# Kernel optimization log

Hardware: AMD Instinct MI355X
Metric: run time of the kernel (lower is better)

The kernel has to match this reference:

```python
import jax, jax.numpy as jnp
import numpy as np

NUM_HEADS = 16
NUM_KV_HEADS = 4
HEAD_DIM = 64
HIDDEN = 1024
B, S = 2, 2048


def setup_inputs() -> dict:
    key = jax.random.key(0)
    ks = jax.random.split(key, 9)
    sc = 0.02
    return {
        "x": jax.random.normal(ks[0], (B, S, HIDDEN), dtype=jnp.float32),
        "Wq": jax.random.normal(ks[1], (HIDDEN, NUM_HEADS * HEAD_DIM), dtype=jnp.float32) * sc,
        "bq": jnp.zeros((NUM_HEADS * HEAD_DIM,), dtype=jnp.float32),
        "Wk": jax.random.normal(ks[2], (HIDDEN, NUM_KV_HEADS * HEAD_DIM), dtype=jnp.float32) * sc,
        "bk": jnp.zeros((NUM_KV_HEADS * HEAD_DIM,), dtype=jnp.float32),
        "Wv": jax.random.normal(ks[3], (HIDDEN, NUM_KV_HEADS * HEAD_DIM), dtype=jnp.float32) * sc,
        "bv": jnp.zeros((NUM_KV_HEADS * HEAD_DIM,), dtype=jnp.float32),
        "Wo": jax.random.normal(ks[4], (NUM_HEADS * HEAD_DIM, HIDDEN), dtype=jnp.float32) * sc,
        "bo": jnp.zeros((HIDDEN,), dtype=jnp.float32),
    }


def reference(x, Wq, bq, Wk, bk, Wv, bv, Wo, bo):
    bs, seq, _ = x.shape
    groups = NUM_HEADS // NUM_KV_HEADS
    # projections -> [B, H, S, D]
    q = (x @ Wq + bq).reshape(bs, seq, NUM_HEADS, HEAD_DIM).transpose(0, 2, 1, 3)
    k = (x @ Wk + bk).reshape(bs, seq, NUM_KV_HEADS, HEAD_DIM).transpose(0, 2, 1, 3)
    v = (x @ Wv + bv).reshape(bs, seq, NUM_KV_HEADS, HEAD_DIM).transpose(0, 2, 1, 3)
    # repeat_interleave KV heads to match query heads (GQA expansion)
    k = jnp.repeat(k, groups, axis=1)
    v = jnp.repeat(v, groups, axis=1)
    # NOTE: source applies NO 1/sqrt(d) scaling and no mask/ALiBi
    scores = jnp.einsum("bhqd,bhkd->bhqk", q, k)
    attn = jax.nn.softmax(scores.astype(jnp.float32), axis=-1).astype(q.dtype)
    out = jnp.einsum("bhqk,bhkd->bhqd", attn, v)
    out = out.transpose(0, 2, 1, 3).reshape(bs, seq, NUM_HEADS * HEAD_DIM)
    return out @ Wo + bo
```

## Files before the change

kernel.cpp:

```cpp
#include <hip/hip_runtime.h>

#define NHEADS 16
#define NKV    4
#define HDIM   64
#define HIDDEN 1024
#define BATCH  2
#define SEQ    2048
#define MROWS  (BATCH * SEQ)
#define LOG2E  1.44269504088896340736f

typedef __bf16 bf16_t;
typedef bf16_t bf16x8 __attribute__((ext_vector_type(8)));
typedef float  f32x4  __attribute__((ext_vector_type(4)));

__device__ __forceinline__ float bf2f(unsigned short u) {
    return __uint_as_float(((unsigned int)u) << 16);
}
__device__ __forceinline__ unsigned short f2bf(float f) {
    unsigned int u = __float_as_uint(f);
    u += 0x7FFFu + ((u >> 16) & 1u);
    return (unsigned short)(u >> 16);
}

__device__ __forceinline__ void gld16(const unsigned short* g, unsigned short* l)
{
    __builtin_amdgcn_global_load_lds(
        (const __attribute__((address_space(1))) void*)g,
        (__attribute__((address_space(3))) void*)l,
        16, 0, 0);
}

__device__ __forceinline__ int swz(int row, int ch) {
    return (row * 8 + (ch ^ (row & 7))) * 8;
}
__device__ __forceinline__ int swz16(int row, int ch) {
    return (row * 16 + (ch ^ (row & 7))) * 8;
}

__global__ void sniff_kernel(const unsigned short* __restrict__ x, int* __restrict__ flag)
{
    const int e = (x[threadIdx.x] >> 7) & 0xFF;
    const unsigned long long ok = __ballot(e >= 110 && e <= 140);
    if (threadIdx.x == 0)
        *flag = (__popcll(ok) < 56) ? 1 : 0;
}

__device__ __forceinline__ void load8cvt(const void* base, size_t elem, bool isf32, unsigned short out[8])
{
    if (!isf32) {
        *(uint4*)out = *(const uint4*)((const unsigned short*)base + elem);
    } else {
        const float* p = (const float*)base + elem;
        float4 v0 = *(const float4*)p;
        float4 v1 = *(const float4*)(p + 4);
        out[0] = f2bf(v0.x); out[1] = f2bf(v0.y); out[2] = f2bf(v0.z); out[3] = f2bf(v0.w);
        out[4] = f2bf(v1.x); out[5] = f2bf(v1.y); out[6] = f2bf(v1.z); out[7] = f2bf(v1.w);
    }
}
__device__ __forceinline__ float bias_at(const void* b, int i, bool isf32)
{
    return isf32 ? ((const float*)b)[i] : bf2f(((const unsigned short*)b)[i]);
}

__global__ __launch_bounds__(256)
void prep_kernel(const void* __restrict__ x,
                 const void* __restrict__ Wq, const void* __restrict__ Wk,
                 const void* __restrict__ Wv, const void* __restrict__ Wo,
                 unsigned short* __restrict__ xb,
                 unsigned short* __restrict__ Wqkvt,
                 unsigned short* __restrict__ Wot,
                 const int* __restrict__ flag)
{
    const bool isf32 = (*flag != 0);
    const int t = threadIdx.x;
    int bid = blockIdx.x;

    if (bid < 2048) {
        if (!isf32) return;
        const size_t c = (size_t)bid * 256 + t;
        unsigned short v[8];
        load8cvt(x, c * 8, true, v);
        *(uint4*)(&xb[c * 8]) = *(uint4*)v;
        return;
    }
    bid -= 2048;
    const void* src; unsigned short* dst; int N, rowoff;
    if (bid < 256)      {             src = Wq; dst = Wqkvt; N = 1024; rowoff = 0;    }
    else if (bid < 320) { bid -= 256; src = Wk; dst = Wqkvt; N = 256;  rowoff = 1024; }
    else if (bid < 384) { bid -= 320; src = Wv; dst = Wqkvt; N = 256;  rowoff = 1280; }
    else                { bid -= 384; src = Wo; dst = Wot;   N = 1024; rowoff = 0;    }
    const int ntx = N / 64;
    const int gn0 = (bid % ntx) * 64;
    const int gk0 = (bid / ntx) * 64;

    __shared__ unsigned short Ts[64][72];
#pragma unroll
    for (int half = 0; half < 2; ++half) {
        const int kl = (t >> 3) + half * 32;
        const int n8 = (t & 7) * 8;
        unsigned short v[8];
        load8cvt(src, (size_t)(gk0 + kl) * N + gn0 + n8, isf32, v);
        *(uint4*)(&Ts[kl][n8]) = *(uint4*)v;
    }
    __syncthreads();
#pragma unroll
    for (int half = 0; half < 2; ++half) {
        const int nl = (t >> 3) + half * 32;
        const int k8 = (t & 7) * 8;
        unsigned short v[8];
#pragma unroll
        for (int j = 0; j < 8; ++j) v[j] = Ts[k8 + j][nl];
        *(uint4*)(&dst[(size_t)(rowoff + gn0 + nl) * HIDDEN + gk0 + k8]) = *(uint4*)v;
    }
}

template<int TBM, int TBN>
__device__ __forceinline__ void gemm_tile(const unsigned short* __restrict__ A,
                                          const unsigned short* __restrict__ Bt,
                                          int K, int m0, int n0,
                                          unsigned short* As, unsigned short* Bs,
                                          f32x4 (&acc)[TBM / 32][TBN / 32])
{
    const int tid  = threadIdx.x;
    const int lane = tid & 63;
    const int wave = tid >> 6;
    const int quad = lane >> 4;
    const int l15  = lane & 15;
    const int wr   = wave >> 1;
    const int wc   = wave & 1;

    for (int k0 = 0; k0 < K; k0 += 128) {
#pragma unroll
        for (int r = 0; r < TBM / 16; ++r) {
            const int u = r * 256 + tid;
            const int row = u >> 4;
            const int gch = ((u & 15) ^ (row & 7)) * 8;
            gld16(&A[(size_t)(m0 + row) * K + k0 + gch], &As[(r * 256 + wave * 64) * 8]);
        }
#pragma unroll
        for (int r = 0; r < TBN / 16; ++r) {
            const int u = r * 256 + tid;
            const int row = u >> 4;
            const int gch = ((u & 15) ^ (row & 7)) * 8;
            gld16(&Bt[(size_t)(n0 + row) * K + k0 + gch], &Bs[(r * 256 + wave * 64) * 8]);
        }
        __syncthreads();

#pragma unroll
        for (int kk = 0; kk < 4; ++kk) {
            bf16x8 af[TBM / 32], bfv[TBN / 32];
#pragma unroll
            for (int i = 0; i < TBM / 32; ++i)
                af[i] = *(const bf16x8*)(&As[swz16(wr * (TBM / 2) + i * 16 + l15, kk * 4 + quad)]);
#pragma unroll
            for (int j = 0; j < TBN / 32; ++j)
                bfv[j] = *(const bf16x8*)(&Bs[swz16(wc * (TBN / 2) + j * 16 + l15, kk * 4 + quad)]);
#pragma unroll
            for (int i = 0; i < TBM / 32; ++i)
#pragma unroll
                for (int j = 0; j < TBN / 32; ++j)
                    acc[i][j] = __builtin_amdgcn_mfma_f32_16x16x32_bf16(af[i], bfv[j], acc[i][j], 0, 0, 0);
        }
        __syncthreads();
    }
}

__global__ __launch_bounds__(256)
void gemm_qkv(const void* __restrict__ xraw,
              const unsigned short* __restrict__ xb,
              const unsigned short* __restrict__ Bt,
              const void* __restrict__ bq, const void* __restrict__ bk,
              const void* __restrict__ bv, const int* __restrict__ flag,
              unsigned short* __restrict__ Qh,
              unsigned short* __restrict__ Kh,
              unsigned short* __restrict__ Vt)
{
    __shared__ __align__(16) unsigned short As[64 * 128];
    __shared__ __align__(16) unsigned short Bs[128 * 128];
    const bool bias_f32 = (*flag != 0);
    const unsigned short* A = bias_f32 ? xb : (const unsigned short*)xraw;
    const int lane = threadIdx.x & 63;
    const int wave = threadIdx.x >> 6;
    const int quad = lane >> 4, l15 = lane & 15;
    const int wr = wave >> 1, wc = wave & 1;
    const int m0 = blockIdx.y * 64, n0 = blockIdx.x * 128;

    f32x4 acc[2][4] = {};
    gemm_tile<64, 128>(A, Bt, HIDDEN, m0, n0, As, Bs, acc);

#pragma unroll
    for (int i = 0; i < 2; ++i) {
#pragma unroll
        for (int j = 0; j < 4; ++j) {
            const int nn  = n0 + wc * 64 + j * 16 + l15;
            const int mmb = m0 + wr * 32 + i * 16 + quad * 4;
            const int b = mmb >> 11, s0 = mmb & 2047;
            if (nn < 1024) {
                const float bias = bias_at(bq, nn, bias_f32);
                const int h = nn >> 6, d = nn & 63;
                const size_t idx0 = (((size_t)(b * NHEADS + h)) * SEQ + s0) * 64 + d;
#pragma unroll
                for (int r = 0; r < 4; ++r)
                    Qh[idx0 + (size_t)r * 64] = f2bf((acc[i][j][r] + bias) * LOG2E);
            } else if (nn < 1280) {
                const int nk = nn - 1024;
                const float bias = bias_at(bk, nk, bias_f32);
                const int h = nk >> 6, d = nk & 63;
                const size_t idx0 = (((size_t)(b * NKV + h)) * SEQ + s0) * 64 + d;
#pragma unroll
                for (int r = 0; r < 4; ++r)
                    Kh[idx0 + (size_t)r * 64] = f2bf(acc[i][j][r] + bias);
            } else {
                const int nv = nn - 1280;
                const float bias = bias_at(bv, nv, bias_f32);
                const int h = nv >> 6, d = nv & 63;
                const size_t idx = (((size_t)(b * NKV + h)) * 64 + d) * SEQ + s0;
                unsigned short vv[4];
#pragma unroll
                for (int r = 0; r < 4; ++r) vv[r] = f2bf(acc[i][j][r] + bias);
                *(uint2*)(&Vt[idx]) = *(uint2*)vv;
            }
        }
    }
}

__global__ __launch_bounds__(256)
void gemm_o(const unsigned short* __restrict__ A,
            const unsigned short* __restrict__ Bt,
            const void* __restrict__ bo, const int* __restrict__ flag,
            float* __restrict__ out)
{
    __shared__ __align__(16) unsigned short As[64 * 128];
    __shared__ __align__(16) unsigned short Bs[128 * 128];
    const bool bias_f32 = (*flag != 0);
    const int lane = threadIdx.x & 63;
    const int wave = threadIdx.x >> 6;
    const int quad = lane >> 4, l15 = lane & 15;
    const int wr = wave >> 1, wc = wave & 1;
    const int m0 = blockIdx.y * 64, n0 = blockIdx.x * 128;

    f32x4 acc[2][4] = {};
    gemm_tile<64, 128>(A, Bt, HIDDEN, m0, n0, As, Bs, acc);

#pragma unroll
    for (int i = 0; i < 2; ++i) {
#pragma unroll
        for (int j = 0; j < 4; ++j) {
            const int nn = n0 + wc * 64 + j * 16 + l15;
            const float bvv = bias_at(bo, nn, bias_f32);
#pragma unroll
            for (int r = 0; r < 4; ++r) {
                const int mm = m0 + wr * 32 + i * 16 + quad * 4 + r;
                out[(size_t)mm * HIDDEN + nn] = acc[i][j][r] + bvv;
            }
        }
    }
}

#define PLD 68
__global__ __launch_bounds__(256)
void attn_kernel(const unsigned short* __restrict__ Qh,
                 const unsigned short* __restrict__ Kh,
                 const unsigned short* __restrict__ Vt,
                 unsigned short* __restrict__ O)
{
    __shared__ __align__(16) unsigned short Kth[64 * 64];
    __shared__ __align__(16) unsigned short VtT[64 * 64];
    __shared__ __align__(16) unsigned short Pt[4][16 * PLD];

    const int tid  = threadIdx.x;
    const int lane = tid & 63;
    const int wave = tid >> 6;
    const int quad = lane >> 4;
    const int l15  = lane & 15;

    const int qt = blockIdx.x;
    const int h  = blockIdx.y;
    const int b  = blockIdx.z;
    const int kv = h >> 2;

    const size_t qoff = ((size_t)(b * NHEADS + h)) * SEQ * HDIM;
    const size_t koff = ((size_t)(b * NKV + kv)) * SEQ * HDIM;
    const size_t voff = ((size_t)(b * NKV + kv)) * HDIM * SEQ;

    const int q0 = qt * 64 + wave * 16;

    const size_t qrow = qoff + (size_t)(q0 + l15) * HDIM;
    const bf16x8 qh0 = *(const bf16x8*)(&Qh[qrow + quad * 8]);
    const bf16x8 qh1 = *(const bf16x8*)(&Qh[qrow + 32 + quad * 8]);

    f32x4 o[4] = {};
    float lsum = 0.0f;

    const int srow0 = tid >> 3;
    const int schp  = tid & 7;

    const unsigned short* Khs = Kh + koff;
    const unsigned short* Vts = Vt + voff;

    for (int kt = 0; kt < SEQ / 64; ++kt, Khs += 64 * HDIM, Vts += 64) {
#pragma unroll
        for (int c = 0; c < 2; ++c) {
            const int row = srow0 + c * 32;
            const int gch = (schp ^ (row & 7)) * 8;
            gld16(&Khs[(size_t)row * 64 + gch],  &Kth[(c * 256 + wave * 64) * 8]);
            gld16(&Vts[(size_t)row * SEQ + gch], &VtT[(c * 256 + wave * 64) * 8]);
        }
        __syncthreads();

        f32x4 s[4];
#pragma unroll
        for (int j = 0; j < 4; ++j) {
            const int rr = j * 16 + l15;
            bf16x8 kh0 = *(const bf16x8*)(&Kth[swz(rr, quad)]);
            bf16x8 kh1 = *(const bf16x8*)(&Kth[swz(rr, quad ^ 4)]);
            f32x4 z = {};
            z = __builtin_amdgcn_mfma_f32_16x16x32_bf16(kh0, qh0, z, 0, 0, 0);
            s[j] = __builtin_amdgcn_mfma_f32_16x16x32_bf16(kh1, qh1, z, 0, 0, 0);
        }

#pragma unroll
        for (int j = 0; j < 4; ++j) {
            unsigned short pb[4];
            float ps = 0.f;
#pragma unroll
            for (int r = 0; r < 4; ++r) {
                const float p = __builtin_amdgcn_exp2f(s[j][r]);
                ps += p;
                pb[r] = f2bf(p);
            }
            lsum += ps;
            *(uint2*)(&Pt[wave][l15 * PLD + j * 16 + quad * 4]) = *(uint2*)pb;
        }

#pragma unroll
        for (int kk = 0; kk < 2; ++kk) {
            bf16x8 pf = *(const bf16x8*)(&Pt[wave][l15 * PLD + kk * 32 + quad * 8]);
#pragma unroll
            for (int dt = 0; dt < 4; ++dt) {
                bf16x8 vf = *(const bf16x8*)(&VtT[swz(dt * 16 + l15, kk * 4 + quad)]);
                o[dt] = __builtin_amdgcn_mfma_f32_16x16x32_bf16(vf, pf, o[dt], 0, 0, 0);
            }
        }
        __syncthreads();
    }

    lsum += __shfl_xor(lsum, 16);
    lsum += __shfl_xor(lsum, 32);

    const float inv = 1.0f / lsum;
    const size_t rowbase = ((size_t)b * SEQ + (q0 + l15)) * (NHEADS * HDIM) + h * HDIM;
#pragma unroll
    for (int dt = 0; dt < 4; ++dt) {
        unsigned short v4[4];
#pragma unroll
        for (int r = 0; r < 4; ++r) v4[r] = f2bf(o[dt][r] * inv);
        *(uint2*)(&O[rowbase + dt * 16 + quad * 4]) = *(uint2*)v4;
    }
}

extern "C" void kernel_launch(void* const* d_in, const int* in_sizes, int n_in,
                              void* d_out, int out_size, void* d_ws, size_t ws_size,
                              hipStream_t stream)
{
    const void* x  = d_in[0];
    const void* Wq = d_in[1];
    const void* bq = d_in[2];
    const void* Wk = d_in[3];
    const void* bk = d_in[4];
    const void* Wv = d_in[5];
    const void* bv = d_in[6];
    const void* Wo = d_in[7];
    const void* bo = d_in[8];
    float* out = (float*)d_out;

    unsigned short* ws = (unsigned short*)d_ws;
    int* flag = (int*)d_ws;
    unsigned short* p = ws + 8;
    unsigned short* xb    = p; p += (size_t)MROWS * HIDDEN;
    unsigned short* Wqkvt = p; p += (size_t)1536 * HIDDEN;
    unsigned short* Wot   = p; p += (size_t)HIDDEN * HIDDEN;
    unsigned short* Qh = p;  p += (size_t)MROWS * 1024;
    unsigned short* Kh = p;  p += (size_t)2 * NKV * SEQ * HDIM;
    unsigned short* Vt = p;  p += (size_t)2 * NKV * SEQ * HDIM;
    unsigned short* A2 = p;  p += (size_t)MROWS * 1024;

    dim3 blk(256);
    sniff_kernel<<<1, 64, 0, stream>>>((const unsigned short*)x, flag);
    prep_kernel<<<dim3(2688), blk, 0, stream>>>(x, Wq, Wk, Wv, Wo, xb, Wqkvt, Wot, flag);
    gemm_qkv<<<dim3(1536 / 128, MROWS / 64), blk, 0, stream>>>(
        x, xb, Wqkvt, bq, bk, bv, flag, Qh, Kh, Vt);
    attn_kernel<<<dim3(SEQ / 64, NHEADS, BATCH), blk, 0, stream>>>(Qh, Kh, Vt, A2);
    gemm_o<<<dim3(1024 / 128, MROWS / 64), blk, 0, stream>>>(A2, Wot, bo, flag, out);
}
```

Measured before the change: 199.5 us.

## Inline dtype sniff, shrink GEMM N-tile to 64, and pack softmax probs with perm

```diff
diff --git a/kernel.cpp b/kernel.cpp
--- a/kernel.cpp
+++ b/kernel.cpp
@@ -37,12 +37,11 @@
     return (row * 16 + (ch ^ (row & 7))) * 8;
 }
 
-__global__ void sniff_kernel(const unsigned short* __restrict__ x, int* __restrict__ flag)
-{
-    const int e = (x[threadIdx.x] >> 7) & 0xFF;
+__device__ __forceinline__ bool sniff_is_f32(const unsigned short* __restrict__ x)
+{
+    const int e = (x[threadIdx.x & 63] >> 7) & 0xFF;
     const unsigned long long ok = __ballot(e >= 110 && e <= 140);
-    if (threadIdx.x == 0)
-        *flag = (__popcll(ok) < 56) ? 1 : 0;
+    return __popcll(ok) < 56;
 }
 
 __device__ __forceinline__ void load8cvt(const void* base, size_t elem, bool isf32, unsigned short out[8])
@@ -68,10 +67,9 @@
                  const void* __restrict__ Wv, const void* __restrict__ Wo,
                  unsigned short* __restrict__ xb,
                  unsigned short* __restrict__ Wqkvt,
-                 unsigned short* __restrict__ Wot,
-                 const int* __restrict__ flag)
-{
-    const bool isf32 = (*flag != 0);
+                 unsigned short* __restrict__ Wot)
+{
+    const bool isf32 = sniff_is_f32((const unsigned short*)x);
     const int t = threadIdx.x;
     int bid = blockIdx.x;
 
@@ -170,29 +168,29 @@
               const unsigned short* __restrict__ xb,
               const unsigned short* __restrict__ Bt,
               const void* __restrict__ bq, const void* __restrict__ bk,
-              const void* __restrict__ bv, const int* __restrict__ flag,
+              const void* __restrict__ bv,
               unsigned short* __restrict__ Qh,
               unsigned short* __restrict__ Kh,
               unsigned short* __restrict__ Vt)
 {
     __shared__ __align__(16) unsigned short As[64 * 128];
-    __shared__ __align__(16) unsigned short Bs[128 * 128];
-    const bool bias_f32 = (*flag != 0);
+    __shared__ __align__(16) unsigned short Bs[64 * 128];
+    const bool bias_f32 = sniff_is_f32((const unsigned short*)xraw);
     const unsigned short* A = bias_f32 ? xb : (const unsigned short*)xraw;
     const int lane = threadIdx.x & 63;
     const int wave = threadIdx.x >> 6;
     const int quad = lane >> 4, l15 = lane & 15;
     const int wr = wave >> 1, wc = wave & 1;
-    const int m0 = blockIdx.y * 64, n0 = blockIdx.x * 128;
-
-    f32x4 acc[2][4] = {};
-    gemm_tile<64, 128>(A, Bt, HIDDEN, m0, n0, As, Bs, acc);
+    const int m0 = blockIdx.y * 64, n0 = blockIdx.x * 64;
+
+    f32x4 acc[2][2] = {};
+    gemm_tile<64, 64>(A, Bt, HIDDEN, m0, n0, As, Bs, acc);
 
 #pragma unroll
     for (int i = 0; i < 2; ++i) {
 #pragma unroll
-        for (int j = 0; j < 4; ++j) {
-            const int nn  = n0 + wc * 64 + j * 16 + l15;
+        for (int j = 0; j < 2; ++j) {
+            const int nn  = n0 + wc * 32 + j * 16 + l15;
             const int mmb = m0 + wr * 32 + i * 16 + quad * 4;
             const int b = mmb >> 11, s0 = mmb & 2047;
             if (nn < 1024) {
@@ -225,28 +223,29 @@
 }
 
 __global__ __launch_bounds__(256)
-void gemm_o(const unsigned short* __restrict__ A,
+void gemm_o(const void* __restrict__ xraw,
+            const unsigned short* __restrict__ A,
             const unsigned short* __restrict__ Bt,
-            const void* __restrict__ bo, const int* __restrict__ flag,
+            const void* __restrict__ bo,
             float* __restrict__ out)
 {
     __shared__ __align__(16) unsigned short As[64 * 128];
-    __shared__ __align__(16) unsigned short Bs[128 * 128];
-    const bool bias_f32 = (*flag != 0);
+    __shared__ __align__(16) unsigned short Bs[64 * 128];
+    const bool bias_f32 = sniff_is_f32((const unsigned short*)xraw);
     const int lane = threadIdx.x & 63;
     const int wave = threadIdx.x >> 6;
     const int quad = lane >> 4, l15 = lane & 15;
     const int wr = wave >> 1, wc = wave & 1;
-    const int m0 = blockIdx.y * 64, n0 = blockIdx.x * 128;
-
-    f32x4 acc[2][4] = {};
-    gemm_tile<64, 128>(A, Bt, HIDDEN, m0, n0, As, Bs, acc);
+    const int m0 = blockIdx.y * 64, n0 = blockIdx.x * 64;
+
+    f32x4 acc[2][2] = {};
+    gemm_tile<64, 64>(A, Bt, HIDDEN, m0, n0, As, Bs, acc);
 
 #pragma unroll
     for (int i = 0; i < 2; ++i) {
 #pragma unroll
-        for (int j = 0; j < 4; ++j) {
-            const int nn = n0 + wc * 64 + j * 16 + l15;
+        for (int j = 0; j < 2; ++j) {
+            const int nn = n0 + wc * 32 + j * 16 + l15;
             const float bvv = bias_at(bo, nn, bias_f32);
 #pragma unroll
             for (int r = 0; r < 4; ++r) {
@@ -321,16 +320,15 @@
 
 #pragma unroll
         for (int j = 0; j < 4; ++j) {
-            unsigned short pb[4];
-            float ps = 0.f;
-#pragma unroll
-            for (int r = 0; r < 4; ++r) {
-                const float p = __builtin_amdgcn_exp2f(s[j][r]);
-                ps += p;
-                pb[r] = f2bf(p);
-            }
-            lsum += ps;
-            *(uint2*)(&Pt[wave][l15 * PLD + j * 16 + quad * 4]) = *(uint2*)pb;
+            const float p0 = __builtin_amdgcn_exp2f(s[j][0]);
+            const float p1 = __builtin_amdgcn_exp2f(s[j][1]);
+            const float p2 = __builtin_amdgcn_exp2f(s[j][2]);
+            const float p3 = __builtin_amdgcn_exp2f(s[j][3]);
+            lsum += (p0 + p1) + (p2 + p3);
+            uint2 w;
+            w.x = __builtin_amdgcn_perm(__float_as_uint(p1), __float_as_uint(p0), 0x07060302u);
+            w.y = __builtin_amdgcn_perm(__float_as_uint(p3), __float_as_uint(p2), 0x07060302u);
+            *(uint2*)(&Pt[wave][l15 * PLD + j * 16 + quad * 4]) = w;
         }
 
 #pragma unroll
@@ -374,9 +372,7 @@
     const void* bo = d_in[8];
     float* out = (float*)d_out;
 
-    unsigned short* ws = (unsigned short*)d_ws;
-    int* flag = (int*)d_ws;
-    unsigned short* p = ws + 8;
+    unsigned short* p = (unsigned short*)d_ws;
     unsigned short* xb    = p; p += (size_t)MROWS * HIDDEN;
     unsigned short* Wqkvt = p; p += (size_t)1536 * HIDDEN;
     unsigned short* Wot   = p; p += (size_t)HIDDEN * HIDDEN;
@@ -386,10 +382,9 @@
     unsigned short* A2 = p;  p += (size_t)MROWS * 1024;
 
     dim3 blk(256);
-    sniff_kernel<<<1, 64, 0, stream>>>((const unsigned short*)x, flag);
-    prep_kernel<<<dim3(2688), blk, 0, stream>>>(x, Wq, Wk, Wv, Wo, xb, Wqkvt, Wot, flag);
-    gemm_qkv<<<dim3(1536 / 128, MROWS / 64), blk, 0, stream>>>(
-        x, xb, Wqkvt, bq, bk, bv, flag, Qh, Kh, Vt);
+    prep_kernel<<<dim3(2688), blk, 0, stream>>>(x, Wq, Wk, Wv, Wo, xb, Wqkvt, Wot);
+    gemm_qkv<<<dim3(1536 / 64, MROWS / 64), blk, 0, stream>>>(
+        x, xb, Wqkvt, bq, bk, bv, Qh, Kh, Vt);
     attn_kernel<<<dim3(SEQ / 64, NHEADS, BATCH), blk, 0, stream>>>(Qh, Kh, Vt, A2);
-    gemm_o<<<dim3(1024 / 128, MROWS / 64), blk, 0, stream>>>(A2, Wot, bo, flag, out);
-}
+    gemm_o<<<dim3(1024 / 64, MROWS / 64), blk, 0, stream>>>(x, A2, Wot, bo, out);
+}
```

Result: faster. 186.5 us (-6.5%).
